# Optimization experiments

Hardware: AMD Instinct MI355X
Metric: run time of the kernel (lower is better)

The kernel has to match this reference:

```python
import jax, jax.numpy as jnp
import numpy as np

# ---- hyperparameters (from pars / init_kwargs) ----
ALPHA = 0.9          # synaptic conductance decay (snn.Synaptic alpha)
BETA = 0.8           # membrane decay (snn.Synaptic beta)
BETA_PLUS = 0.9      # pre-synaptic trace decay
BETA_MINUS = 0.9     # post-synaptic trace decay
THRESHOLD = 1.0
W_MIN, W_MAX = 0.0, 1.0
A_PLUS, A_MINUS = 0.008, 0.0008
T, B, IN, N = 350, 128, 784, 400
SPIKE_P = 0.05       # Bernoulli firing probability of the rate-coded input


def setup_inputs() -> dict:
    key = jax.random.key(0)
    k_img, k_w = jax.random.split(key)
    # Poisson/Bernoulli rate-coded MNIST spike train [T, B, IN]
    image = (jax.random.uniform(k_img, (T, B, IN)) < SPIKE_P).astype(jnp.float32)
    # nn.Linear default init U(-1/sqrt(IN), 1/sqrt(IN)) then clamp to [w_min, w_max]
    s = 1.0 / np.sqrt(IN)
    W = jnp.clip(jax.random.uniform(k_w, (N, IN), minval=-s, maxval=s), W_MIN, W_MAX)
    return {"image": image, "W": W}


def reference(image, W):
    """Fused LIF (snntorch Synaptic, reset-by-subtraction) + STDP loop over T steps.

    Returns (W_final, mem_final, syn_final, total_spikes_per_neuron).
    """
    batch = image.shape[1]

    def step(carry, x_t):
        syn, mem, pre_tr, post_tr, W = carry
        # pre-synaptic trace: tr_t = beta_plus * tr_{t-1} + x_t
        pre_tr = BETA_PLUS * pre_tr + x_t                      # [B, IN]
        # linear projection (no bias)
        I_t = jnp.einsum('bi,ni->bn', x_t, W)                  # [B, N]
        # snntorch Synaptic: reset from pre-update mem, subtract mechanism
        reset = (mem > THRESHOLD).astype(mem.dtype)
        syn = ALPHA * syn + I_t
        mem = BETA * mem + syn - reset * THRESHOLD
        spk = (mem > THRESHOLD).astype(mem.dtype)              # [B, N]
        # post-synaptic trace
        post_tr = BETA_MINUS * post_tr + spk
        # STDP: potentiate on post spike x pre trace, depress on pre spike x post trace
        dW = (A_PLUS * jnp.einsum('bn,bi->ni', spk, pre_tr)
              - A_MINUS * jnp.einsum('bn,bi->ni', post_tr, x_t)) / batch
        W = jnp.clip(W + dW, W_MIN, W_MAX)
        return (syn, mem, pre_tr, post_tr, W), spk.sum(axis=0)

    syn0 = jnp.zeros((batch, N), image.dtype)
    mem0 = jnp.zeros((batch, N), image.dtype)
    pre0 = jnp.zeros((batch, IN), image.dtype)
    post0 = jnp.zeros((batch, N), image.dtype)

    (syn, mem, _, _, W_final), spk_counts = jax.lax.scan(
        step, (syn0, mem0, pre0, post0, W), image)
    return W_final, mem, syn, spk_counts.sum(axis=0)
```

## Files before the change

kernel.cpp:

```cpp
#include <hip/hip_runtime.h>
#include <hip/hip_bf16.h>


#define TT    350
#define BB    128
#define INF   784
#define NNEU  400
#define NS    2
#define NTHR  1024
#define LCAP  80

#define ALPHA 0.9f
#define BETA  0.8f
#define BPLUS 0.9f
#define BMIN  0.9f
#define CP    (0.008f/128.0f)
#define CM    (0.0008f/128.0f)

__device__ __forceinline__ float bf2f(__hip_bfloat16 v){ return __bfloat162float(v); }

__device__ __forceinline__ void barx(){
  asm volatile("s_waitcnt lgkmcnt(0)" ::: "memory");
  __builtin_amdgcn_s_barrier();
  __builtin_amdgcn_sched_barrier(0);
}

__device__ __forceinline__ float dppred(float x){
  x += __int_as_float(__builtin_amdgcn_update_dpp(0, __float_as_int(x), 0x4E,  0xF, 0xF, true));
  x += __int_as_float(__builtin_amdgcn_update_dpp(0, __float_as_int(x), 0x124, 0xF, 0xF, true));
  x += __int_as_float(__builtin_amdgcn_update_dpp(0, __float_as_int(x), 0x128, 0xF, 0xF, true));
  return x;
}

__global__ void k_pretr(const float* __restrict__ img, __hip_bfloat16* __restrict__ pre){
  int idx = blockIdx.x*blockDim.x + threadIdx.x;
  if (idx >= BB*INF) return;
  float v = 0.f;
  for (int t=0;t<TT;t++){
    v = BPLUS*v + img[(size_t)t*(BB*INF) + idx];
    pre[(size_t)t*(BB*INF) + idx] = __float2bfloat16(v);
  }
}

__global__ void k_masks(const float* __restrict__ img,
                        unsigned short* __restrict__ lists,
                        int* __restrict__ cnts,
                        unsigned int* __restrict__ collist,
                        ulonglong2* __restrict__ rawcm){
  __shared__ unsigned long long rowbits[BB][13];
  __shared__ unsigned short buf[16][LCAP];
  const int t = blockIdx.x;
  const int tid = threadIdx.x, lane = tid & 63, w = tid >> 6;
  const float* base = img + (size_t)t*(BB*INF);

  for (int r8=0; r8<8; r8++){
    int r = w*8 + r8;
    const float* p = base + (size_t)r*INF;
    for (int c=0;c<13;c++){
      int i = c*64 + lane;
      bool a = (i < INF) && (p[i] > 0.f);
      unsigned long long bal = __ballot(a);
      if (lane == 0) rowbits[r][c] = bal;
    }
  }
  for (int r8=0; r8<8; r8++){
    int r = w*8 + r8;
    int cnt = 0;
    for (int c=0;c<13;c++){
      unsigned long long word = rowbits[r][c];
      int i = c*64 + lane;
      bool a = (word >> lane) & 1ull;
      int pos = cnt + __popcll(word & ((1ull<<lane)-1ull));
      if (a && pos < LCAP) buf[w][pos] = (unsigned short)(i<<3);
      cnt += __popcll(word);
    }
    for (int k = cnt + lane; k < LCAP; k += 64) buf[w][k] = (unsigned short)(INF<<3);
    if (lane == 0) cnts[t*BB + r] = (cnt < LCAP) ? cnt : LCAP;
    if (lane < LCAP/2)
      ((unsigned int*)(lists + (size_t)(t*BB + r)*LCAP))[lane] = ((unsigned int*)buf[w])[lane];
  }
  __syncthreads();
  if (tid < INF){
    int wsel = tid >> 6, bit = tid & 63;
    unsigned long long m0=0, m1=0;
    for (int b=0;b<64;b++) m0 |= ((rowbits[b][wsel]    >> bit) & 1ull) << b;
    for (int b=0;b<64;b++) m1 |= ((rowbits[64+b][wsel] >> bit) & 1ull) << b;
    ulonglong2 rm; rm.x = m0; rm.y = m1;
    rawcm[(size_t)t*INF + tid] = rm;
    int cnt = __popcll(m0) + __popcll(m1);
    unsigned int wd[8];
    wd[0] = (unsigned int)cnt; wd[1]=0;wd[2]=0;wd[3]=0;wd[4]=0;wd[5]=0;wd[6]=0;wd[7]=0;
    #pragma unroll
    for (int k=1;k<32;k++){
      int bb;
      if (m0){ bb = __builtin_ctzll(m0); m0 &= m0-1; }
      else if (m1){ bb = 64 + __builtin_ctzll(m1); m1 &= m1-1; }
      else bb = 128;
      wd[k>>2] |= ((unsigned int)bb) << ((k&3)*8);
    }
    uint4* dst = (uint4*)(collist + ((size_t)t*INF + tid)*8);
    uint4 lo; lo.x=wd[0]; lo.y=wd[1]; lo.z=wd[2]; lo.w=wd[3];
    uint4 hi; hi.x=wd[4]; hi.y=wd[5]; hi.z=wd[6]; hi.w=wd[7];
    dst[0]=lo; dst[1]=hi;
  }
}

#define G2(W) { float2 a_ = *(const float2*)((const char*)&Wp2[0] + ((W) & 0xffffu)); I0 += a_.x; I1 += a_.y; \
                float2 b_ = *(const float2*)((const char*)&Wp2[0] + ((W) >> 16));     I0 += b_.x; I1 += b_.y; }
#define GATHER8(V) { G2((V).x); G2((V).y); G2((V).z); G2((V).w); }

#define DEP4(W) { float2 p_; \
  p_ = postl[(W) & 0xffu];        d0 += p_.x; d1 += p_.y; \
  p_ = postl[((W)>>8) & 0xffu];   d0 += p_.x; d1 += p_.y; \
  p_ = postl[((W)>>16) & 0xffu];  d0 += p_.x; d1 += p_.y; \
  p_ = postl[(W)>>24];            d0 += p_.x; d1 += p_.y; }

__launch_bounds__(NTHR, 1)
__global__ void k_main(const float* __restrict__ Win,
                       const __hip_bfloat16* __restrict__ pre,
                       const unsigned short* __restrict__ lists,
                       const int* __restrict__ cnts,
                       const unsigned int* __restrict__ collist,
                       const ulonglong2* __restrict__ rawcm,
                       float* __restrict__ out){
  __shared__ float2 Wp2[800];
  __shared__ float2 postl[132];
  __shared__ unsigned long long smQ[2][2];
  __shared__ float cntS[2];

  const int tid  = threadIdx.x;
  const int lane = tid & 63;
  const int wv   = tid >> 6;
  const int q    = (lane >> 1) & 7;
  const int b    = (lane & 1) | (((lane >> 4) & 3) << 1) | (wv << 3);
  const int n0   = blockIdx.x * NS;

  if (tid < 800){
    float2 w;
    w.x = (tid < INF) ? Win[(size_t)n0*INF + tid] : 0.f;
    w.y = (tid < INF) ? Win[(size_t)(n0+1)*INF + tid] : 0.f;
    Wp2[tid] = w;
  }
  if (tid < 132){ postl[tid].x = 0.f; postl[tid].y = 0.f; }
  if (tid < 2) cntS[tid] = 0.f;

  const int  c0   = tid;
  const bool hasc = (c0 < INF);

  float syn0=0.f, mem0=0.f, syn1=0.f, mem1=0.f, sc0=0.f, sc1=0.f;
  float potR0=0.f, potR1=0.f;
  unsigned long long p00=0ull, p01=0ull, p10=0ull, p11=0ull;
  bool anyEver = false;

  uint4 lA = *(const uint4*)(lists + ((size_t)b)*LCAP + (size_t)q*8);
  int cn = cnts[b];
  uint4 cl0; cl0.x=0;cl0.y=0;cl0.z=0;cl0.w=0;
  ulonglong2 cm0; cm0.x=0; cm0.y=0;
  if (hasc){ cl0 = *(const uint4*)(collist + (size_t)c0*8); cm0 = rawcm[c0]; }

  __syncthreads();

  for (int t=0; t<TT; t++){
    float I0 = 0.f, I1 = 0.f;
    GATHER8(lA);
    if (cn > 64 + q*8){
      uint4 lC = *(const uint4*)(lists + ((size_t)t*BB + b)*LCAP + 64 + (size_t)q*8);
      GATHER8(lC);
    }
    int tn = (t+1 < TT) ? t+1 : TT-1;
    uint4 lAn = *(const uint4*)(lists + ((size_t)tn*BB + b)*LCAP + (size_t)q*8);
    int cnn = cnts[tn*BB + b];
    uint4 cl0n = cl0; ulonglong2 cm0n = cm0;
    if (hasc){
      cl0n = *(const uint4*)(collist + ((size_t)tn*INF + c0)*8);
      cm0n = rawcm[(size_t)tn*INF + c0];
    }

    I0 = dppred(I0);
    I1 = dppred(I1);

    float r0 = (mem0 > 1.f) ? 1.f : 0.f;
    syn0 = ALPHA*syn0 + I0;
    mem0 = BETA*mem0 + syn0 - r0;
    float s0 = (mem0 > 1.f) ? 1.f : 0.f;
    float r1 = (mem1 > 1.f) ? 1.f : 0.f;
    syn1 = ALPHA*syn1 + I1;
    mem1 = BETA*mem1 + syn1 - r1;
    float s1 = (mem1 > 1.f) ? 1.f : 0.f;
    unsigned long long bal0 = __ballot(s0 > 0.5f);
    unsigned long long bal1 = __ballot(s1 > 0.5f);
    if (q == 0){
      sc0 += s0; sc1 += s1;
      float2 pv = postl[b];
      pv.x = BMIN*pv.x + s0;
      pv.y = BMIN*pv.y + s1;
      postl[b] = pv;
    }
    if (lane == 0){
      unsigned int by0 = (unsigned int)((bal0 & 3ull) | ((bal0>>16)&3ull)<<2 |
                                        ((bal0>>32)&3ull)<<4 | ((bal0>>48)&3ull)<<6);
      unsigned int by1 = (unsigned int)((bal1 & 3ull) | ((bal1>>16)&3ull)<<2 |
                                        ((bal1>>32)&3ull)<<4 | ((bal1>>48)&3ull)<<6);
      ((unsigned char*)smQ)[wv]      = (unsigned char)by0;
      ((unsigned char*)smQ)[16 + wv] = (unsigned char)by1;
    }
    barx();

    unsigned long long s00 = smQ[0][0], s01 = smQ[0][1];
    unsigned long long s10 = smQ[1][0], s11 = smQ[1][1];
    bool anyNow = ((s00|s01|s10|s11) != 0ull);
    bool runD = anyEver || anyNow;
    anyEver = runD;

    if (runD && hasc){
      float d0=0.f, d1=0.f;
      unsigned int w0_ = cl0.x;
      { float2 p_;
        p_ = postl[(w0_>>8) & 0xffu];  d0 += p_.x; d1 += p_.y;
        p_ = postl[(w0_>>16) & 0xffu]; d0 += p_.x; d1 += p_.y;
        p_ = postl[w0_>>24];           d0 += p_.x; d1 += p_.y; }
      DEP4(cl0.y); DEP4(cl0.z); DEP4(cl0.w);
      int cc_ = (int)(w0_ & 0xffu);
      if (cc_ > 15){
        uint4 e2_ = *(const uint4*)(collist + ((size_t)t*INF + c0)*8 + 4);
        DEP4(e2_.x); DEP4(e2_.y); DEP4(e2_.z); DEP4(e2_.w);
      }
      float pot0 = BPLUS*potR0 + (float)(__popcll(cm0.x & p00) + __popcll(cm0.y & p01));
      float pot1 = BPLUS*potR1 + (float)(__popcll(cm0.x & p10) + __popcll(cm0.y & p11));
      unsigned long long f00 = (s00^p00) & cm0.x, f01 = (s01^p01) & cm0.y;
      unsigned long long f10 = (s10^p10) & cm0.x, f11 = (s11^p11) & cm0.y;
      if (f00|f01|f10|f11){
        const __hip_bfloat16* prow = pre + (size_t)t*(BB*INF) + c0;
        while (f00){ int bb=__builtin_ctzll(f00); f00&=f00-1;
          float v=bf2f(prow[(size_t)bb*INF]);      pot0 += ((s00>>bb)&1ull)? v : -v; }
        while (f01){ int bb=__builtin_ctzll(f01); f01&=f01-1;
          float v=bf2f(prow[(size_t)(64+bb)*INF]); pot0 += ((s01>>bb)&1ull)? v : -v; }
        while (f10){ int bb=__builtin_ctzll(f10); f10&=f10-1;
          float v=bf2f(prow[(size_t)bb*INF]);      pot1 += ((s10>>bb)&1ull)? v : -v; }
        while (f11){ int bb=__builtin_ctzll(f11); f11&=f11-1;
          float v=bf2f(prow[(size_t)(64+bb)*INF]); pot1 += ((s11>>bb)&1ull)? v : -v; }
      }
      potR0 = pot0; potR1 = pot1;
      float2 wv_ = Wp2[c0];
      wv_.x = fminf(fmaxf(wv_.x + CP*pot0 - CM*d0, 0.f), 1.f);
      wv_.y = fminf(fmaxf(wv_.y + CP*pot1 - CM*d1, 0.f), 1.f);
      Wp2[c0] = wv_;
    }
    p00=s00; p01=s01; p10=s10; p11=s11;

    lA=lAn; cn=cnn; cl0=cl0n; cm0=cm0n;
    barx();
  }

  __syncthreads();
  if (tid < INF){
    float2 wvv = Wp2[tid];
    out[(size_t)n0*INF + tid]       = wvv.x;
    out[(size_t)(n0+1)*INF + tid]   = wvv.y;
  }
  if (q == 0){
    out[(size_t)NNEU*INF + (size_t)b*NNEU + n0]                        = mem0;
    out[(size_t)NNEU*INF + (size_t)b*NNEU + n0 + 1]                    = mem1;
    out[(size_t)NNEU*INF + (size_t)BB*NNEU + (size_t)b*NNEU + n0]      = syn0;
    out[(size_t)NNEU*INF + (size_t)BB*NNEU + (size_t)b*NNEU + n0 + 1]  = syn1;
    atomicAdd(&cntS[0], sc0);
    atomicAdd(&cntS[1], sc1);
  }
  __syncthreads();
  if (tid < 2) out[(size_t)NNEU*INF + 2*(size_t)BB*NNEU + n0 + tid] = cntS[tid];
}

extern "C" void kernel_launch(void* const* d_in, const int* in_sizes, int n_in,
                              void* d_out, int out_size, void* d_ws, size_t ws_size,
                              hipStream_t stream) {
  const float* img = (const float*)d_in[0];
  const float* W   = (const float*)d_in[1];
  float* out = (float*)d_out;

  char* ws = (char*)d_ws;
  __hip_bfloat16* pre  = (__hip_bfloat16*)ws;
  unsigned short* lst  = (unsigned short*)(ws + 70246400);
  int*            cnts = (int*)(ws + 77414400);
  unsigned int*   coll = (unsigned int*)(ws + 77593600);
  ulonglong2*     rcm  = (ulonglong2*)(ws + 86374400);

  k_pretr<<<(BB*INF + 255)/256, 256, 0, stream>>>(img, pre);
  k_masks<<<TT, NTHR, 0, stream>>>(img, lst, cnts, coll, rcm);
  k_main <<<NNEU/NS, NTHR, 0, stream>>>(W, pre, lst, cnts, coll, rcm, out);
}
```

Before: 785.0 us.

## Exit STDP loop early once weights saturate and replace per-column lists

Adds a runtime check that all of a block's weights have clamped to 1.0 and that every neuron is pinned spiking. From that step on, it finishes the LIF recurrence in closed form from per-row spike counts and skips the gather and STDP work. Two precompute kernels supply the per-column trace sums and a step index after which potentiation always outweighs depression, which guards the exit. Depression now uses a shared post-trace plus a sparse correction over rows whose trace differs, and potentiation sums the complement when more than half the batch spiked. The cost is extra preprocessing passes and barriers, and exactness depends on the saturation guards holding.

```diff
diff --git a/kernel.cpp b/kernel.cpp
--- a/kernel.cpp
+++ b/kernel.cpp
@@ -32,8 +32,10 @@
   return x;
 }
 
-__global__ void k_pretr(const float* __restrict__ img, __hip_bfloat16* __restrict__ pre){
+__global__ void k_pretr(const float* __restrict__ img, __hip_bfloat16* __restrict__ pre,
+                        int* __restrict__ minRowA){
   int idx = blockIdx.x*blockDim.x + threadIdx.x;
+  if (idx < BB) minRowA[idx] = 0x7fffffff;
   if (idx >= BB*INF) return;
   float v = 0.f;
   for (int t=0;t<TT;t++){
@@ -42,11 +44,23 @@
   }
 }
 
+__global__ void k_S(const __hip_bfloat16* __restrict__ pre, float* __restrict__ S,
+                    int* __restrict__ safe_from){
+  int idx = blockIdx.x*blockDim.x + threadIdx.x;
+  if (idx == 0) *safe_from = 0;
+  if (idx >= TT*INF) return;
+  int t = idx / INF, i = idx - t*INF;
+  const __hip_bfloat16* p = pre + (size_t)t*(BB*INF) + i;
+  float s = 0.f;
+  for (int b=0;b<BB;b++) s += bf2f(p[(size_t)b*INF]);
+  S[idx] = s;
+}
+
 __global__ void k_masks(const float* __restrict__ img,
                         unsigned short* __restrict__ lists,
                         int* __restrict__ cnts,
-                        unsigned int* __restrict__ collist,
-                        ulonglong2* __restrict__ rawcm){
+                        ulonglong2* __restrict__ rawcm,
+                        int* __restrict__ minRowA){
   __shared__ unsigned long long rowbits[BB][13];
   __shared__ unsigned short buf[16][LCAP];
   const int t = blockIdx.x;
@@ -75,7 +89,11 @@
       cnt += __popcll(word);
     }
     for (int k = cnt + lane; k < LCAP; k += 64) buf[w][k] = (unsigned short)(INF<<3);
-    if (lane == 0) cnts[t*BB + r] = (cnt < LCAP) ? cnt : LCAP;
+    if (lane == 0){
+      int cv = (cnt < LCAP) ? cnt : LCAP;
+      cnts[t*BB + r] = cv;
+      atomicMin(&minRowA[r], cv);
+    }
     if (lane < LCAP/2)
       ((unsigned int*)(lists + (size_t)(t*BB + r)*LCAP))[lane] = ((unsigned int*)buf[w])[lane];
   }
@@ -87,46 +105,53 @@
     for (int b=0;b<64;b++) m1 |= ((rowbits[64+b][wsel] >> bit) & 1ull) << b;
     ulonglong2 rm; rm.x = m0; rm.y = m1;
     rawcm[(size_t)t*INF + tid] = rm;
-    int cnt = __popcll(m0) + __popcll(m1);
-    unsigned int wd[8];
-    wd[0] = (unsigned int)cnt; wd[1]=0;wd[2]=0;wd[3]=0;wd[4]=0;wd[5]=0;wd[6]=0;wd[7]=0;
-    #pragma unroll
-    for (int k=1;k<32;k++){
-      int bb;
-      if (m0){ bb = __builtin_ctzll(m0); m0 &= m0-1; }
-      else if (m1){ bb = 64 + __builtin_ctzll(m1); m1 &= m1-1; }
-      else bb = 128;
-      wd[k>>2] |= ((unsigned int)bb) << ((k&3)*8);
-    }
-    uint4* dst = (uint4*)(collist + ((size_t)t*INF + tid)*8);
-    uint4 lo; lo.x=wd[0]; lo.y=wd[1]; lo.z=wd[2]; lo.w=wd[3];
-    uint4 hi; hi.x=wd[4]; hi.y=wd[5]; hi.z=wd[6]; hi.w=wd[7];
-    dst[0]=lo; dst[1]=hi;
-  }
+  }
+}
+
+__global__ void k_safe(const float* __restrict__ S, const ulonglong2* __restrict__ rcm,
+                       int* __restrict__ safe_from){
+  int t = blockIdx.x, i = threadIdx.x;
+  bool bad = false;
+  if (i < INF){
+    ulonglong2 m = rcm[(size_t)t*INF + i];
+    float cntf = (float)(__popcll(m.x) + __popcll(m.y));
+    bad = !(S[(size_t)t*INF + i] >= cntf + 0.5f);
+  }
+  if (bad) atomicMax(safe_from, t+1);
+}
+
+__device__ __forceinline__ float potf(unsigned long long ma, unsigned long long mb,
+                                      int pc, float Sv,
+                                      const __hip_bfloat16* __restrict__ prt, int c){
+  bool direct = (pc <= 64);
+  unsigned long long m = direct ? ma : ~ma;
+  unsigned long long n = direct ? mb : ~mb;
+  float acc = 0.f;
+  while (m){ int bb = __builtin_ctzll(m); m &= m-1; acc += bf2f(prt[(size_t)bb*INF + c]); }
+  while (n){ int bb = __builtin_ctzll(n); n &= n-1; acc += bf2f(prt[(size_t)(64+bb)*INF + c]); }
+  return direct ? acc : (Sv - acc);
 }
 
 #define G2(W) { float2 a_ = *(const float2*)((const char*)&Wp2[0] + ((W) & 0xffffu)); I0 += a_.x; I1 += a_.y; \
                 float2 b_ = *(const float2*)((const char*)&Wp2[0] + ((W) >> 16));     I0 += b_.x; I1 += b_.y; }
 #define GATHER8(V) { G2((V).x); G2((V).y); G2((V).z); G2((V).w); }
 
-#define DEP4(W) { float2 p_; \
-  p_ = postl[(W) & 0xffu];        d0 += p_.x; d1 += p_.y; \
-  p_ = postl[((W)>>8) & 0xffu];   d0 += p_.x; d1 += p_.y; \
-  p_ = postl[((W)>>16) & 0xffu];  d0 += p_.x; d1 += p_.y; \
-  p_ = postl[(W)>>24];            d0 += p_.x; d1 += p_.y; }
-
 __launch_bounds__(NTHR, 1)
 __global__ void k_main(const float* __restrict__ Win,
                        const __hip_bfloat16* __restrict__ pre,
+                       const float* __restrict__ S,
                        const unsigned short* __restrict__ lists,
                        const int* __restrict__ cnts,
-                       const unsigned int* __restrict__ collist,
                        const ulonglong2* __restrict__ rawcm,
+                       const int* __restrict__ minRowA,
+                       const int* __restrict__ safe_fromP,
                        float* __restrict__ out){
   __shared__ float2 Wp2[800];
   __shared__ float2 postl[132];
   __shared__ unsigned long long smQ[2][2];
+  __shared__ ulonglong2 mdiffL[2];
   __shared__ float cntS[2];
+  __shared__ unsigned pinw[2];
 
   const int tid  = threadIdx.x;
   const int lane = tid & 63;
@@ -142,21 +167,27 @@
     Wp2[tid] = w;
   }
   if (tid < 132){ postl[tid].x = 0.f; postl[tid].y = 0.f; }
-  if (tid < 2) cntS[tid] = 0.f;
+  if (tid < 2){ cntS[tid] = 0.f; pinw[tid] = 0xFFFFu; }
+  if (tid == 0){
+    mdiffL[0].x = 0ull; mdiffL[0].y = 0ull;
+    mdiffL[1].x = 0ull; mdiffL[1].y = 0ull;
+  }
 
   const int  c0   = tid;
   const bool hasc = (c0 < INF);
+  const int  mR   = minRowA[b];
+  const int  sfrom = *safe_fromP;
 
   float syn0=0.f, mem0=0.f, syn1=0.f, mem1=0.f, sc0=0.f, sc1=0.f;
-  float potR0=0.f, potR1=0.f;
-  unsigned long long p00=0ull, p01=0ull, p10=0ull, p11=0ull;
+  float C0=0.f, C1=0.f;
   bool anyEver = false;
+  int tres = TT;
 
   uint4 lA = *(const uint4*)(lists + ((size_t)b)*LCAP + (size_t)q*8);
   int cn = cnts[b];
-  uint4 cl0; cl0.x=0;cl0.y=0;cl0.z=0;cl0.w=0;
   ulonglong2 cm0; cm0.x=0; cm0.y=0;
-  if (hasc){ cl0 = *(const uint4*)(collist + (size_t)c0*8); cm0 = rawcm[c0]; }
+  float sv0 = 0.f;
+  if (hasc){ cm0 = rawcm[c0]; sv0 = S[c0]; }
 
   __syncthreads();
 
@@ -170,10 +201,10 @@
     int tn = (t+1 < TT) ? t+1 : TT-1;
     uint4 lAn = *(const uint4*)(lists + ((size_t)tn*BB + b)*LCAP + (size_t)q*8);
     int cnn = cnts[tn*BB + b];
-    uint4 cl0n = cl0; ulonglong2 cm0n = cm0;
+    ulonglong2 cm0n = cm0; float sv0n = sv0;
     if (hasc){
-      cl0n = *(const uint4*)(collist + ((size_t)tn*INF + c0)*8);
       cm0n = rawcm[(size_t)tn*INF + c0];
+      sv0n = S[tn*INF + c0];
     }
 
     I0 = dppred(I0);
@@ -192,8 +223,8 @@
     if (q == 0){
       sc0 += s0; sc1 += s1;
       float2 pv = postl[b];
-      pv.x = BMIN*pv.x + s0;
-      pv.y = BMIN*pv.y + s1;
+      pv.x = fmaf(BMIN, pv.x, s0);
+      pv.y = fmaf(BMIN, pv.y, s1);
       postl[b] = pv;
     }
     if (lane == 0){
@@ -208,48 +239,82 @@
 
     unsigned long long s00 = smQ[0][0], s01 = smQ[0][1];
     unsigned long long s10 = smQ[1][0], s11 = smQ[1][1];
+    float sb0 = (float)(int)(s00 & 1ull);
+    float sb1 = (float)(int)(s10 & 1ull);
+    C0 = fmaf(BMIN, C0, sb0);
+    C1 = fmaf(BMIN, C1, sb1);
+    ulonglong2 mdv = mdiffL[t & 1];
+    unsigned long long sf0 = (s00 & 1ull) ? ~s00 : s00;
+    unsigned long long sf1 = (s00 & 1ull) ? ~s01 : s01;
+    unsigned long long sg0 = (s10 & 1ull) ? ~s10 : s10;
+    unsigned long long sg1 = (s10 & 1ull) ? ~s11 : s11;
+    unsigned long long md0 = mdv.x | sf0 | sg0;
+    unsigned long long md1 = mdv.y | sf1 | sg1;
+
     bool anyNow = ((s00|s01|s10|s11) != 0ull);
     bool runD = anyEver || anyNow;
     anyEver = runD;
 
+    if (wv == 13){
+      float2 a0 = postl[lane], a1 = postl[64 + lane];
+      bool eq0 = (a0.x == C0) && (a0.y == C1);
+      bool eq1 = (a1.x == C0) && (a1.y == C1);
+      unsigned long long d0 = ~__ballot(eq0);
+      unsigned long long d1 = ~__ballot(eq1);
+      if (lane == 0){ mdiffL[(t+1)&1].x = d0; mdiffL[(t+1)&1].y = d1; }
+    }
+
+    bool wok;
     if (runD && hasc){
-      float d0=0.f, d1=0.f;
-      unsigned int w0_ = cl0.x;
-      { float2 p_;
-        p_ = postl[(w0_>>8) & 0xffu];  d0 += p_.x; d1 += p_.y;
-        p_ = postl[(w0_>>16) & 0xffu]; d0 += p_.x; d1 += p_.y;
-        p_ = postl[w0_>>24];           d0 += p_.x; d1 += p_.y; }
-      DEP4(cl0.y); DEP4(cl0.z); DEP4(cl0.w);
-      int cc_ = (int)(w0_ & 0xffu);
-      if (cc_ > 15){
-        uint4 e2_ = *(const uint4*)(collist + ((size_t)t*INF + c0)*8 + 4);
-        DEP4(e2_.x); DEP4(e2_.y); DEP4(e2_.z); DEP4(e2_.w);
-      }
-      float pot0 = BPLUS*potR0 + (float)(__popcll(cm0.x & p00) + __popcll(cm0.y & p01));
-      float pot1 = BPLUS*potR1 + (float)(__popcll(cm0.x & p10) + __popcll(cm0.y & p11));
-      unsigned long long f00 = (s00^p00) & cm0.x, f01 = (s01^p01) & cm0.y;
-      unsigned long long f10 = (s10^p10) & cm0.x, f11 = (s11^p11) & cm0.y;
-      if (f00|f01|f10|f11){
-        const __hip_bfloat16* prow = pre + (size_t)t*(BB*INF) + c0;
-        while (f00){ int bb=__builtin_ctzll(f00); f00&=f00-1;
-          float v=bf2f(prow[(size_t)bb*INF]);      pot0 += ((s00>>bb)&1ull)? v : -v; }
-        while (f01){ int bb=__builtin_ctzll(f01); f01&=f01-1;
-          float v=bf2f(prow[(size_t)(64+bb)*INF]); pot0 += ((s01>>bb)&1ull)? v : -v; }
-        while (f10){ int bb=__builtin_ctzll(f10); f10&=f10-1;
-          float v=bf2f(prow[(size_t)bb*INF]);      pot1 += ((s10>>bb)&1ull)? v : -v; }
-        while (f11){ int bb=__builtin_ctzll(f11); f11&=f11-1;
-          float v=bf2f(prow[(size_t)(64+bb)*INF]); pot1 += ((s11>>bb)&1ull)? v : -v; }
-      }
-      potR0 = pot0; potR1 = pot1;
+      float cntf = (float)(__popcll(cm0.x) + __popcll(cm0.y));
+      float dep0 = C0 * cntf, dep1 = C1 * cntf;
+      unsigned long long g0 = md0 & cm0.x, g1 = md1 & cm0.y;
+      while (g0){ int bb = __builtin_ctzll(g0); g0 &= g0-1;
+        float2 p_ = postl[bb];      dep0 += p_.x - C0; dep1 += p_.y - C1; }
+      while (g1){ int bb = __builtin_ctzll(g1); g1 &= g1-1;
+        float2 p_ = postl[64+bb];   dep0 += p_.x - C0; dep1 += p_.y - C1; }
+      int pc0 = __popcll(s00) + __popcll(s01);
+      int pc1 = __popcll(s10) + __popcll(s11);
+      const __hip_bfloat16* prt = pre + (size_t)t*(BB*INF);
+      float pot0 = potf(s00, s01, pc0, sv0, prt, c0);
+      float pot1 = potf(s10, s11, pc1, sv0, prt, c0);
       float2 wv_ = Wp2[c0];
-      wv_.x = fminf(fmaxf(wv_.x + CP*pot0 - CM*d0, 0.f), 1.f);
-      wv_.y = fminf(fmaxf(wv_.y + CP*pot1 - CM*d1, 0.f), 1.f);
+      wv_.x = fminf(fmaxf(wv_.x + CP*pot0 - CM*dep0, 0.f), 1.f);
+      wv_.y = fminf(fmaxf(wv_.y + CP*pot1 - CM*dep1, 0.f), 1.f);
       Wp2[c0] = wv_;
-    }
-    p00=s00; p01=s01; p10=s10; p11=s11;
-
-    lA=lAn; cn=cnn; cl0=cl0n; cm0=cm0n;
+      wok = (wv_.x == 1.0f) && (wv_.y == 1.0f);
+    } else {
+      wok = !hasc;
+    }
+
+    bool mypin = runD && wok && (syn0 >= 2.0f) && (syn1 >= 2.0f) && (mR >= 2);
+    unsigned long long bp = __ballot(mypin);
+    if (lane == 0){
+      if (bp != ~0ull) atomicAnd(&pinw[t & 1], ~(1u << wv));
+      pinw[(t+1) & 1] = 0xFFFFu;
+    }
+
+    lA=lAn; cn=cnn; cm0=cm0n; sv0=sv0n;
     barx();
+
+    if (pinw[t & 1] == 0xFFFFu && (t+1) >= sfrom){ tres = t+1; break; }
+  }
+
+  if (tres < TT){
+    float Ic = (float)cnts[tres*BB + b];
+    for (int tt = tres; tt < TT; ++tt){
+      float In = (tt+1 < TT) ? (float)cnts[(tt+1)*BB + b] : 0.f;
+      float r0 = (mem0 > 1.f) ? 1.f : 0.f;
+      syn0 = ALPHA*syn0 + Ic;
+      mem0 = BETA*mem0 + syn0 - r0;
+      float s0 = (mem0 > 1.f) ? 1.f : 0.f;
+      float r1 = (mem1 > 1.f) ? 1.f : 0.f;
+      syn1 = ALPHA*syn1 + Ic;
+      mem1 = BETA*mem1 + syn1 - r1;
+      float s1 = (mem1 > 1.f) ? 1.f : 0.f;
+      sc0 += s0; sc1 += s1;
+      Ic = In;
+    }
   }
 
   __syncthreads();
@@ -279,12 +344,16 @@
 
   char* ws = (char*)d_ws;
   __hip_bfloat16* pre  = (__hip_bfloat16*)ws;
-  unsigned short* lst  = (unsigned short*)(ws + 70246400);
-  int*            cnts = (int*)(ws + 77414400);
-  unsigned int*   coll = (unsigned int*)(ws + 77593600);
-  ulonglong2*     rcm  = (ulonglong2*)(ws + 86374400);
-
-  k_pretr<<<(BB*INF + 255)/256, 256, 0, stream>>>(img, pre);
-  k_masks<<<TT, NTHR, 0, stream>>>(img, lst, cnts, coll, rcm);
-  k_main <<<NNEU/NS, NTHR, 0, stream>>>(W, pre, lst, cnts, coll, rcm, out);
-}
+  float*          S    = (float*)(ws + 70246400);
+  unsigned short* lst  = (unsigned short*)(ws + 71344000);
+  int*            cnts = (int*)(ws + 78512000);
+  ulonglong2*     rcm  = (ulonglong2*)(ws + 78691200);
+  int*            mrw  = (int*)(ws + 83081600);
+  int*            sfp  = (int*)(ws + 83082112);
+
+  k_pretr<<<(BB*INF + 255)/256, 256, 0, stream>>>(img, pre, mrw);
+  k_masks<<<TT, NTHR, 0, stream>>>(img, lst, cnts, rcm, mrw);
+  k_S    <<<(TT*INF + 255)/256, 256, 0, stream>>>(pre, S, sfp);
+  k_safe <<<TT, NTHR, 0, stream>>>(S, rcm, sfp);
+  k_main <<<NNEU/NS, NTHR, 0, stream>>>(W, pre, S, lst, cnts, rcm, mrw, sfp, out);
+}
```

Result: slower. 931.7 us (+18.7%).
